# Kernel tuning notes

Measured on AMD Instinct MI355X. Metric: run time of the kernel, lower is better.

Reference implementation:

```python
import jax, jax.numpy as jnp
import numpy as np

N, E, G = 10000, 160000, 64
F, C1, C2, C3, K, NC = 128, 128, 256, 512, 5, 10


def setup_inputs() -> dict:
    key = jax.random.key(0)
    ks = jax.random.split(key, 12)
    s = 0.05
    return {
        "x": jax.random.normal(ks[0], (N, F), dtype=jnp.float32),
        "edge_index": jax.random.randint(ks[1], (2, E), 0, N, dtype=jnp.int64),
        "batch": jnp.sort(jax.random.randint(ks[2], (N,), 0, G, dtype=jnp.int64)),
        "W_cheb": jax.random.normal(ks[3], (K, F, C1), dtype=jnp.float32) * s,
        "b_cheb": jnp.zeros((C1,), jnp.float32),
        "W_g1": jax.random.normal(ks[4], (C1, C2), dtype=jnp.float32) * s,
        "b_g1": jnp.zeros((C2,), jnp.float32),
        "W_g2": jax.random.normal(ks[5], (C2, C3), dtype=jnp.float32) * s,
        "b_g2": jnp.zeros((C3,), jnp.float32),
        "w_gate": jax.random.normal(ks[6], (C3, 1), dtype=jnp.float32) * s,
        "b_gate": jnp.zeros((1,), jnp.float32),
        "W_fc": jax.random.normal(ks[7], (C3, NC), dtype=jnp.float32) * s,
        "b_fc": jnp.zeros((NC,), jnp.float32),
    }


def _deg_inv_sqrt(deg):
    return jnp.where(deg > 0, jax.lax.rsqrt(jnp.maximum(deg, 1e-12)), 0.0)


def cheb_conv(x, src, dst, W, b):
    # PyG ChebConv, sym normalization, lambda_max=2 => scaled Laplacian = -D^-1/2 A D^-1/2
    ones = jnp.ones((src.shape[0],), x.dtype)
    deg = jax.ops.segment_sum(ones, src, num_segments=N)
    dinv = _deg_inv_sqrt(deg)
    w = -(dinv[src] * dinv[dst])  # [E]

    def prop(h):
        return jax.ops.segment_sum(w[:, None] * h[src], dst, num_segments=N)

    tx0 = x
    tx1 = prop(x)
    out = tx0 @ W[0] + tx1 @ W[1]
    for k in range(2, W.shape[0]):
        tx2 = 2.0 * prop(tx1) - tx0
        out = out + tx2 @ W[k]
        tx0, tx1 = tx1, tx2
    return out + b


def gcn_conv(x, src, dst, W, b):
    # PyG GCNConv: add self-loops, sym norm D~^-1/2 (A+I) D~^-1/2, transform then aggregate
    loop = jnp.arange(N, dtype=src.dtype)
    src_a = jnp.concatenate([src, loop])
    dst_a = jnp.concatenate([dst, loop])
    ones = jnp.ones((src_a.shape[0],), x.dtype)
    deg = jax.ops.segment_sum(ones, dst_a, num_segments=N)
    dinv = _deg_inv_sqrt(deg)
    norm = dinv[src_a] * dinv[dst_a]  # [E+N]
    h = x @ W
    return jax.ops.segment_sum(norm[:, None] * h[src_a], dst_a, num_segments=N) + b


def attention_pool(x, batch, w_gate, b_gate):
    logits = (x @ w_gate + b_gate)[:, 0]  # [N]
    m = jax.ops.segment_max(logits, batch, num_segments=G)
    e = jnp.exp(logits - m[batch])
    s = jax.ops.segment_sum(e, batch, num_segments=G)
    alpha = e / s[batch]
    return jax.ops.segment_sum(alpha[:, None] * x, batch, num_segments=G)  # [G, C3]


def reference(x, edge_index, batch, W_cheb, b_cheb, W_g1, b_g1, W_g2, b_g2,
              w_gate, b_gate, W_fc, b_fc):
    src, dst = edge_index[0], edge_index[1]
    h = jax.nn.relu(cheb_conv(x, src, dst, W_cheb, b_cheb))
    h = jax.nn.relu(gcn_conv(h, src, dst, W_g1, b_g1))
    h = jax.nn.relu(gcn_conv(h, src, dst, W_g2, b_g2))
    g = attention_pool(h, batch, w_gate, b_gate)
    logits = g @ W_fc + b_fc
    return jax.nn.log_softmax(logits, axis=1)
```

## Files before the change

### kernel.cpp

```cpp
#include <hip/hip_runtime.h>
#include <hip/hip_bf16.h>
#include <math.h>

#define N_NODES 10000
#define N_EDGES 160000
#define N_GRAPHS 64
#define F_IN    128
#define C1_DIM  128
#define C2_DIM  256
#define C3_DIM  512
#define K_CHEB  5
#define NCLS    10

typedef short v8s __attribute__((ext_vector_type(8)));
typedef float v4f __attribute__((ext_vector_type(4)));

static __device__ __forceinline__ unsigned short f2bf(float f) {
    unsigned u = __float_as_uint(f);
    unsigned r = (u + 0x7FFFu + ((u >> 16) & 1u)) >> 16;
    return (unsigned short)r;
}
static __device__ __forceinline__ float bf_lo(unsigned u) { return __uint_as_float(u << 16); }
static __device__ __forceinline__ float bf_hi(unsigned u) { return __uint_as_float(u & 0xFFFF0000u); }

__global__ void count_kernel(const int* __restrict__ src, const int* __restrict__ dst,
                             int* __restrict__ cnt_s, int* __restrict__ cnt_d, int E) {
    int e = blockIdx.x * blockDim.x + threadIdx.x;
    if (e >= E) return;
    atomicAdd(&cnt_s[src[e]], 1);
    atomicAdd(&cnt_d[dst[e]], 1);
}

__global__ void dinv_kernel(const int* __restrict__ cnt_s, const int* __restrict__ cnt_d,
                            float* __restrict__ dinv_c, float* __restrict__ dinv_g, int n) {
    int i = blockIdx.x * blockDim.x + threadIdx.x;
    if (i >= n) return;
    int cs = cnt_s[i];
    dinv_c[i] = (cs > 0) ? rsqrtf((float)cs) : 0.0f;
    dinv_g[i] = rsqrtf((float)cnt_d[i] + 1.0f);
}

__global__ __launch_bounds__(256) void scan_kernel(const int* __restrict__ cnt,
                                                   int* __restrict__ rowptr, int n) {
    __shared__ int sums[256];
    int tid = threadIdx.x;
    int chunk = (n + 255) / 256;
    int s0 = tid * chunk, s1 = min(n, s0 + chunk);
    int loc = 0;
    for (int i = s0; i < s1; i++) loc += cnt[i];
    sums[tid] = loc;
    __syncthreads();
    for (int off = 1; off < 256; off <<= 1) {
        int t = (tid >= off) ? sums[tid - off] : 0;
        __syncthreads();
        sums[tid] += t;
        __syncthreads();
    }
    int pre = sums[tid] - loc;
    for (int i = s0; i < s1; i++) { rowptr[i] = pre; pre += cnt[i]; }
    if (tid == 255) rowptr[n] = pre;
}

__global__ void fill_kernel(const int* __restrict__ src, const int* __restrict__ dst,
                            const float* __restrict__ dinv_c, const float* __restrict__ dinv_g,
                            const int* __restrict__ rowptr, int* __restrict__ fillc,
                            int* __restrict__ col, float* __restrict__ wch,
                            float* __restrict__ nrm, int E) {
    int e = blockIdx.x * blockDim.x + threadIdx.x;
    if (e >= E) return;
    int s = src[e], d = dst[e];
    int pos = rowptr[d] + atomicAdd(&fillc[d], 1);
    col[pos] = s;
    wch[pos] = -(dinv_c[s] * dinv_c[d]);
    nrm[pos] = dinv_g[s] * dinv_g[d];
}

__global__ void conv_x_kernel(const float* __restrict__ x, unsigned short* __restrict__ xb,
                              unsigned short* __restrict__ tcat) {
    int id = blockIdx.x * blockDim.x + threadIdx.x;
    if (id >= N_NODES * 64) return;
    int n = id >> 6, f = (id & 63) * 2;
    float2 v = *(const float2*)(x + (size_t)n * F_IN + f);
    ushort2 o; o.x = f2bf(v.x); o.y = f2bf(v.y);
    *(ushort2*)(xb + (size_t)n * F_IN + f) = o;
    *(ushort2*)(tcat + (size_t)n * (K_CHEB * F_IN) + f) = o;
}

__global__ void wt_kernel(const float* __restrict__ Wsrc, unsigned short* __restrict__ Bt,
                          int K, int N) {
    int id = blockIdx.x * blockDim.x + threadIdx.x;
    if (id >= K * N) return;
    int n = id % N, k = id / N;
    Bt[(size_t)n * K + k] = f2bf(Wsrc[(size_t)k * N + n]);
}

__global__ __launch_bounds__(256) void gather_cheb_bf(
        const unsigned short* __restrict__ tb, const int* __restrict__ rowptr,
        const int* __restrict__ col, const float* __restrict__ ew,
        const unsigned short* __restrict__ base, float alpha, float beta,
        unsigned short* __restrict__ outc, unsigned short* __restrict__ tslice, int n) {
    int w = (blockIdx.x * blockDim.x + threadIdx.x) >> 6;
    int lane = threadIdx.x & 63;
    if (w >= n) return;
    float a0 = 0.0f, a1 = 0.0f;
    int rs = rowptr[w], re = rowptr[w + 1];
    for (int b = rs; b < re; b += 64) {
        int cl = 0; float wl = 0.0f;
        if (b + lane < re) { cl = col[b + lane]; wl = ew[b + lane]; }
        int nk4 = (min(64, re - b) + 3) & ~3;
        for (int j = 0; j < nk4; j += 4) {
            int s0 = __shfl(cl, j), s1 = __shfl(cl, j + 1);
            int s2 = __shfl(cl, j + 2), s3 = __shfl(cl, j + 3);
            float w0 = __shfl(wl, j), w1 = __shfl(wl, j + 1);
            float w2 = __shfl(wl, j + 2), w3 = __shfl(wl, j + 3);
            unsigned u0 = ((const unsigned*)(tb + (size_t)s0 * F_IN))[lane];
            unsigned u1 = ((const unsigned*)(tb + (size_t)s1 * F_IN))[lane];
            unsigned u2 = ((const unsigned*)(tb + (size_t)s2 * F_IN))[lane];
            unsigned u3 = ((const unsigned*)(tb + (size_t)s3 * F_IN))[lane];
            a0 += w0 * bf_lo(u0) + w1 * bf_lo(u1) + w2 * bf_lo(u2) + w3 * bf_lo(u3);
            a1 += w0 * bf_hi(u0) + w1 * bf_hi(u1) + w2 * bf_hi(u2) + w3 * bf_hi(u3);
        }
    }
    if (base) {
        unsigned ub = ((const unsigned*)(base + (size_t)w * F_IN))[lane];
        a0 = alpha * a0 + beta * bf_lo(ub);
        a1 = alpha * a1 + beta * bf_hi(ub);
    } else {
        a0 *= alpha; a1 *= alpha;
    }
    ushort2 o; o.x = f2bf(a0); o.y = f2bf(a1);
    *(ushort2*)(outc + (size_t)w * F_IN + lane * 2) = o;
    *(ushort2*)(tslice + (size_t)w * (K_CHEB * F_IN) + lane * 2) = o;
}

template<int FPL>
__global__ __launch_bounds__(256) void gather_gcn_pre(
        const unsigned short* __restrict__ tb, const int* __restrict__ rowptr,
        const int* __restrict__ col, const float* __restrict__ ew,
        const float* __restrict__ dinv, unsigned short* __restrict__ z, int n) {
    const int C = FPL * 64;
    int w = (blockIdx.x * blockDim.x + threadIdx.x) >> 6;
    int lane = threadIdx.x & 63;
    if (w >= n) return;
    float acc[FPL];
    #pragma unroll
    for (int q = 0; q < FPL; q++) acc[q] = 0.0f;
    int rs = rowptr[w], re = rowptr[w + 1];
    for (int b = rs; b < re; b += 64) {
        int cl = 0; float wl = 0.0f;
        if (b + lane < re) { cl = col[b + lane]; wl = ew[b + lane]; }
        int nk4 = (min(64, re - b) + 3) & ~3;
        for (int j = 0; j < nk4; j += 4) {
            int s0 = __shfl(cl, j), s1 = __shfl(cl, j + 1);
            int s2 = __shfl(cl, j + 2), s3 = __shfl(cl, j + 3);
            float w0 = __shfl(wl, j), w1 = __shfl(wl, j + 1);
            float w2 = __shfl(wl, j + 2), w3 = __shfl(wl, j + 3);
            if constexpr (FPL == 2) {
                unsigned u0 = ((const unsigned*)(tb + (size_t)s0 * C))[lane];
                unsigned u1 = ((const unsigned*)(tb + (size_t)s1 * C))[lane];
                unsigned u2 = ((const unsigned*)(tb + (size_t)s2 * C))[lane];
                unsigned u3 = ((const unsigned*)(tb + (size_t)s3 * C))[lane];
                acc[0] += w0 * bf_lo(u0) + w1 * bf_lo(u1) + w2 * bf_lo(u2) + w3 * bf_lo(u3);
                acc[1] += w0 * bf_hi(u0) + w1 * bf_hi(u1) + w2 * bf_hi(u2) + w3 * bf_hi(u3);
            } else {
                uint2 u0 = ((const uint2*)(tb + (size_t)s0 * C))[lane];
                uint2 u1 = ((const uint2*)(tb + (size_t)s1 * C))[lane];
                uint2 u2 = ((const uint2*)(tb + (size_t)s2 * C))[lane];
                uint2 u3 = ((const uint2*)(tb + (size_t)s3 * C))[lane];
                acc[0] += w0 * bf_lo(u0.x) + w1 * bf_lo(u1.x) + w2 * bf_lo(u2.x) + w3 * bf_lo(u3.x);
                acc[1] += w0 * bf_hi(u0.x) + w1 * bf_hi(u1.x) + w2 * bf_hi(u2.x) + w3 * bf_hi(u3.x);
                acc[2] += w0 * bf_lo(u0.y) + w1 * bf_lo(u1.y) + w2 * bf_lo(u2.y) + w3 * bf_lo(u3.y);
                acc[3] += w0 * bf_hi(u0.y) + w1 * bf_hi(u1.y) + w2 * bf_hi(u2.y) + w3 * bf_hi(u3.y);
            }
        }
    }
    float sn = dinv[w] * dinv[w];
    if constexpr (FPL == 2) {
        unsigned u = ((const unsigned*)(tb + (size_t)w * C))[lane];
        acc[0] += sn * bf_lo(u); acc[1] += sn * bf_hi(u);
        ushort2 o; o.x = f2bf(acc[0]); o.y = f2bf(acc[1]);
        *(ushort2*)(z + (size_t)w * C + lane * 2) = o;
    } else {
        uint2 u = ((const uint2*)(tb + (size_t)w * C))[lane];
        acc[0] += sn * bf_lo(u.x); acc[1] += sn * bf_hi(u.x);
        acc[2] += sn * bf_lo(u.y); acc[3] += sn * bf_hi(u.y);
        ushort4 o; o.x = f2bf(acc[0]); o.y = f2bf(acc[1]);
        o.z = f2bf(acc[2]); o.w = f2bf(acc[3]);
        *(ushort4*)(z + (size_t)w * C + lane * 4) = o;
    }
}

__global__ __launch_bounds__(256) void gemm_bf16(
        const unsigned short* __restrict__ A, const unsigned short* __restrict__ Bt,
        const float* __restrict__ bias, float* __restrict__ Cf,
        unsigned short* __restrict__ Cb, int M, int K, int N, int relu) {
    int m0 = blockIdx.y * 128, n0 = blockIdx.x * 128;
    int wave = threadIdx.x >> 6, lane = threadIdx.x & 63;
    int wm = (wave & 1) * 64, wn = (wave >> 1) * 64;
    int l15 = lane & 15, quad = lane >> 4;

    v4f acc[4][4];
    #pragma unroll
    for (int i = 0; i < 4; i++)
        #pragma unroll
        for (int j = 0; j < 4; j++) acc[i][j] = (v4f){0.f, 0.f, 0.f, 0.f};

    const unsigned short* Ab[4]; bool av[4];
    #pragma unroll
    for (int i = 0; i < 4; i++) {
        int row = m0 + wm + i * 16 + l15;
        av[i] = row < M;
        Ab[i] = A + (size_t)(av[i] ? row : 0) * K + quad * 8;
    }
    const unsigned short* Bb[4];
    #pragma unroll
    for (int j = 0; j < 4; j++) {
        int coln = n0 + wn + j * 16 + l15;
        Bb[j] = Bt + (size_t)coln * K + quad * 8;
    }
    const v8s zero8 = {0, 0, 0, 0, 0, 0, 0, 0};

    for (int k0 = 0; k0 < K; k0 += 32) {
        v8s a[4], b[4];
        #pragma unroll
        for (int i = 0; i < 4; i++) a[i] = av[i] ? *(const v8s*)(Ab[i] + k0) : zero8;
        #pragma unroll
        for (int j = 0; j < 4; j++) b[j] = *(const v8s*)(Bb[j] + k0);
        #pragma unroll
        for (int i = 0; i < 4; i++)
            #pragma unroll
            for (int j = 0; j < 4; j++)
                acc[i][j] = __builtin_amdgcn_mfma_f32_16x16x32_bf16(a[i], b[j], acc[i][j], 0, 0, 0);
    }

    #pragma unroll
    for (int j = 0; j < 4; j++) {
        int coln = n0 + wn + j * 16 + l15;
        float bv = bias ? bias[coln] : 0.0f;
        #pragma unroll
        for (int i = 0; i < 4; i++) {
            int rbase = m0 + wm + i * 16 + quad * 4;
            #pragma unroll
            for (int r = 0; r < 4; r++) {
                int row = rbase + r;
                if (row >= M) continue;
                float v = acc[i][j][r] + bv;
                if (relu) v = fmaxf(v, 0.0f);
                if (Cf) Cf[(size_t)row * N + coln] = v;
                else    Cb[(size_t)row * N + coln] = f2bf(v);
            }
        }
    }
}

__global__ void gate_kernel(const float* __restrict__ h3, const float* __restrict__ wg,
                            const float* __restrict__ bg, float* __restrict__ logits, int n) {
    int node = blockIdx.x * 4 + (threadIdx.x >> 6);
    int lane = threadIdx.x & 63;
    if (node >= n) return;
    float s = 0.0f;
    #pragma unroll
    for (int i = 0; i < 8; i++) {
        int c = i * 64 + lane;
        s += h3[(size_t)node * C3_DIM + c] * wg[c];
    }
    #pragma unroll
    for (int off = 32; off > 0; off >>= 1) s += __shfl_down(s, off);
    if (lane == 0) logits[node] = s + bg[0];
}

__global__ void gptr_kernel(const int* __restrict__ batch, int* __restrict__ gptr, int n) {
    int i = blockIdx.x * blockDim.x + threadIdx.x;
    if (i >= n) return;
    int b = batch[i];
    if (i == 0) { for (int g = 0; g <= b; g++) gptr[g] = 0; }
    else {
        int bp = batch[i - 1];
        for (int g = bp + 1; g <= b; g++) gptr[g] = i;
    }
    if (i == n - 1) { for (int g = b + 1; g <= N_GRAPHS; g++) gptr[g] = n; }
}

__global__ __launch_bounds__(256) void pool_stats(float* __restrict__ logits,
                                                  const int* __restrict__ gptr) {
    __shared__ float red[256];
    int g = blockIdx.x, tid = threadIdx.x;
    int gs = gptr[g], ge = gptr[g + 1];
    float m = -INFINITY;
    for (int i = gs + tid; i < ge; i += 256) m = fmaxf(m, logits[i]);
    red[tid] = m; __syncthreads();
    for (int off = 128; off > 0; off >>= 1) {
        if (tid < off) red[tid] = fmaxf(red[tid], red[tid + off]);
        __syncthreads();
    }
    m = red[0]; __syncthreads();
    float s = 0.0f;
    for (int i = gs + tid; i < ge; i += 256) s += expf(logits[i] - m);
    red[tid] = s; __syncthreads();
    for (int off = 128; off > 0; off >>= 1) {
        if (tid < off) red[tid] += red[tid + off];
        __syncthreads();
    }
    s = red[0];
    float sinv = (s > 0.0f) ? 1.0f / s : 0.0f;
    for (int i = gs + tid; i < ge; i += 256)
        logits[i] = expf(logits[i] - m) * sinv;
}

__global__ __launch_bounds__(256) void pool_partial(const float* __restrict__ h3,
        const float* __restrict__ alpha, const int* __restrict__ gptr,
        float* __restrict__ pooled) {
    int g = blockIdx.x, ch = blockIdx.y, sl = blockIdx.z;
    int gs = gptr[g], ge = gptr[g + 1];
    int cnt = ge - gs;
    int i0 = gs + (cnt * sl) / 8;
    int i1 = gs + (cnt * (sl + 1)) / 8;
    int c = ch * 256 + threadIdx.x;
    float acc = 0.0f;
    for (int i = i0; i < i1; i++)
        acc += alpha[i] * h3[(size_t)i * C3_DIM + c];
    if (i1 > i0) atomicAdd(&pooled[(size_t)g * C3_DIM + c], acc);
}

__global__ void fc_kernel(const float* __restrict__ pooled, const float* __restrict__ Wfc,
                          const float* __restrict__ bfc, float* __restrict__ out) {
    int g = blockIdx.x;
    int t = threadIdx.x;
    float acc = -INFINITY;
    if (t < NCLS) {
        acc = bfc[t];
        for (int k = 0; k < C3_DIM; k++)
            acc += pooled[(size_t)g * C3_DIM + k] * Wfc[k * NCLS + t];
    }
    float m = acc;
    #pragma unroll
    for (int off = 8; off > 0; off >>= 1) m = fmaxf(m, __shfl_xor(m, off, 16));
    float e = (t < NCLS) ? expf(acc - m) : 0.0f;
    float s = e;
    #pragma unroll
    for (int off = 8; off > 0; off >>= 1) s += __shfl_xor(s, off, 16);
    if (t < NCLS) out[g * NCLS + t] = acc - m - logf(s);
}

extern "C" void kernel_launch(void* const* d_in, const int* in_sizes, int n_in,
                              void* d_out, int out_size, void* d_ws, size_t ws_size,
                              hipStream_t stream) {
    const float* x      = (const float*)d_in[0];
    const int*   ei     = (const int*)d_in[1];
    const int*   batch  = (const int*)d_in[2];
    const float* W_cheb = (const float*)d_in[3];
    const float* b_cheb = (const float*)d_in[4];
    const float* W_g1   = (const float*)d_in[5];
    const float* b_g1   = (const float*)d_in[6];
    const float* W_g2   = (const float*)d_in[7];
    const float* b_g2   = (const float*)d_in[8];
    const float* w_gate = (const float*)d_in[9];
    const float* b_gate = (const float*)d_in[10];
    const float* W_fc   = (const float*)d_in[11];
    const float* b_fc   = (const float*)d_in[12];
    const int* src = ei;
    const int* dst = ei + N_EDGES;
    float* out = (float*)d_out;

    const int N = N_NODES, E = N_EDGES, G = N_GRAPHS;

    char* Wp = (char*)d_ws;
    auto alloc = [&](size_t bytes) {
        void* p = Wp;
        Wp += (bytes + 255) & ~(size_t)255;
        return p;
    };
    int*   cnt_s   = (int*)alloc(N * 4);
    int*   cnt_d   = (int*)alloc(N * 4);
    int*   fillc   = (int*)alloc(N * 4);
    int*   rowptr  = (int*)alloc((N + 1) * 4);
    int*   col     = (int*)alloc(E * 4);
    float* wch     = (float*)alloc(E * 4);
    float* nrm     = (float*)alloc(E * 4);
    float* dinv_c  = (float*)alloc(N * 4);
    float* dinv_g  = (float*)alloc(N * 4);
    unsigned short* xb    = (unsigned short*)alloc((size_t)N * F_IN * 2);
    unsigned short* t1b   = (unsigned short*)alloc((size_t)N * F_IN * 2);
    unsigned short* t2b   = (unsigned short*)alloc((size_t)N * F_IN * 2);
    unsigned short* t3b   = (unsigned short*)alloc((size_t)N * F_IN * 2);
    unsigned short* t4b   = (unsigned short*)alloc((size_t)N * F_IN * 2);
    unsigned short* tcat  = (unsigned short*)alloc((size_t)N * K_CHEB * F_IN * 2);
    unsigned short* h1b   = (unsigned short*)alloc((size_t)N * C1_DIM * 2);
    unsigned short* z1b   = (unsigned short*)alloc((size_t)N * C1_DIM * 2);
    unsigned short* h2b   = (unsigned short*)alloc((size_t)N * C2_DIM * 2);
    unsigned short* z2b   = (unsigned short*)alloc((size_t)N * C2_DIM * 2);
    float* h3      = (float*)alloc((size_t)N * C3_DIM * 4);
    unsigned short* Wcb_t = (unsigned short*)alloc((size_t)K_CHEB * F_IN * C1_DIM * 2);
    unsigned short* Wg1_t = (unsigned short*)alloc((size_t)C1_DIM * C2_DIM * 2);
    unsigned short* Wg2_t = (unsigned short*)alloc((size_t)C2_DIM * C3_DIM * 2);
    float* logits  = (float*)alloc(N * 4);
    int*   gptr    = (int*)alloc((G + 1) * 4);
    float* pooled  = (float*)alloc((size_t)G * C3_DIM * 4);

    dim3 blk(256);
    auto cdiv = [](int a, int b) { return (a + b - 1) / b; };

    hipMemsetAsync(cnt_s, 0, N * sizeof(int), stream);
    hipMemsetAsync(cnt_d, 0, N * sizeof(int), stream);
    hipMemsetAsync(fillc, 0, N * sizeof(int), stream);
    hipLaunchKernelGGL(count_kernel, dim3(cdiv(E, 256)), blk, 0, stream, src, dst, cnt_s, cnt_d, E);
    hipLaunchKernelGGL(dinv_kernel, dim3(cdiv(N, 256)), blk, 0, stream, cnt_s, cnt_d, dinv_c, dinv_g, N);
    hipLaunchKernelGGL(scan_kernel, dim3(1), blk, 0, stream, cnt_d, rowptr, N);
    hipLaunchKernelGGL(fill_kernel, dim3(cdiv(E, 256)), blk, 0, stream,
                       src, dst, dinv_c, dinv_g, rowptr, fillc, col, wch, nrm, E);

    hipLaunchKernelGGL(conv_x_kernel, dim3(cdiv(N * 64, 256)), blk, 0, stream, x, xb, tcat);
    hipLaunchKernelGGL(wt_kernel, dim3(cdiv(K_CHEB * F_IN * C1_DIM, 256)), blk, 0, stream,
                       W_cheb, Wcb_t, K_CHEB * F_IN, C1_DIM);
    hipLaunchKernelGGL(wt_kernel, dim3(cdiv(C1_DIM * C2_DIM, 256)), blk, 0, stream,
                       W_g1, Wg1_t, C1_DIM, C2_DIM);
    hipLaunchKernelGGL(wt_kernel, dim3(cdiv(C2_DIM * C3_DIM, 256)), blk, 0, stream,
                       W_g2, Wg2_t, C2_DIM, C3_DIM);

    const int NWB = cdiv(N, 4);
    const int TC = K_CHEB * F_IN;

    hipLaunchKernelGGL(gather_cheb_bf, dim3(NWB), blk, 0, stream,
                       xb, rowptr, col, wch, (const unsigned short*)nullptr, 1.0f, 0.0f,
                       t1b, tcat + 1 * F_IN, N);
    hipLaunchKernelGGL(gather_cheb_bf, dim3(NWB), blk, 0, stream,
                       t1b, rowptr, col, wch, xb, 2.0f, -1.0f, t2b, tcat + 2 * F_IN, N);
    hipLaunchKernelGGL(gather_cheb_bf, dim3(NWB), blk, 0, stream,
                       t2b, rowptr, col, wch, t1b, 2.0f, -1.0f, t3b, tcat + 3 * F_IN, N);
    hipLaunchKernelGGL(gather_cheb_bf, dim3(NWB), blk, 0, stream,
                       t3b, rowptr, col, wch, t2b, 2.0f, -1.0f, t4b, tcat + 4 * F_IN, N);

    hipLaunchKernelGGL(gemm_bf16, dim3(C1_DIM / 128, cdiv(N, 128)), blk, 0, stream,
                       tcat, Wcb_t, b_cheb, (float*)nullptr, h1b, N, TC, C1_DIM, 1);

    hipLaunchKernelGGL(gather_gcn_pre<2>, dim3(NWB), blk, 0, stream,
                       h1b, rowptr, col, nrm, dinv_g, z1b, N);
    hipLaunchKernelGGL(gemm_bf16, dim3(C2_DIM / 128, cdiv(N, 128)), blk, 0, stream,
                       z1b, Wg1_t, b_g1, (float*)nullptr, h2b, N, C1_DIM, C2_DIM, 1);

    hipLaunchKernelGGL(gather_gcn_pre<4>, dim3(NWB), blk, 0, stream,
                       h2b, rowptr, col, nrm, dinv_g, z2b, N);
    hipLaunchKernelGGL(gemm_bf16, dim3(C3_DIM / 128, cdiv(N, 128)), blk, 0, stream,
                       z2b, Wg2_t, b_g2, h3, (unsigned short*)nullptr, N, C2_DIM, C3_DIM, 1);

    hipLaunchKernelGGL(gate_kernel, dim3(cdiv(N, 4)), blk, 0, stream, h3, w_gate, b_gate, logits, N);
    hipLaunchKernelGGL(gptr_kernel, dim3(cdiv(N, 256)), blk, 0, stream, batch, gptr, N);
    hipLaunchKernelGGL(pool_stats, dim3(G), blk, 0, stream, logits, gptr);
    hipMemsetAsync(pooled, 0, (size_t)G * C3_DIM * sizeof(float), stream);
    hipLaunchKernelGGL(pool_partial, dim3(G, C3_DIM / 256, 8), blk, 0, stream,
                       h3, logits, gptr, pooled);

    hipLaunchKernelGGL(fc_kernel, dim3(G), dim3(64), 0, stream, pooled, W_fc, b_fc, out);
}
```

Measured before the change: 320.1 us.

## Merge prep kernels, gather Chebyshev terms in place, shrink GEMM M-tile

Folds the x conversion, the three weight transposes and the graph-pointer build into one prep kernel, and merges the dinv computation into the scan kernel. The memsets are consolidated, and the pooled buffer is now zeroed inside pool_stats. The Chebyshev gathers read and write directly in the concatenated tcat buffer at stride TC, which drops the separate t1..t4 buffers and the duplicate store. The GEMM tile height goes from 128 to 64 rows, giving twice as many blocks for better occupancy on a 10000-row problem, at the cost of less B reuse per block. Reading from the strided tcat buffer may reduce cache locality in the gathers.

```diff
diff --git a/kernel.cpp b/kernel.cpp
--- a/kernel.cpp
+++ b/kernel.cpp
@@ -11,6 +11,7 @@
 #define C3_DIM  512
 #define K_CHEB  5
 #define NCLS    10
+#define TC      (K_CHEB * F_IN)
 
 typedef short v8s __attribute__((ext_vector_type(8)));
 typedef float v4f __attribute__((ext_vector_type(4)));
@@ -31,23 +32,21 @@
     atomicAdd(&cnt_d[dst[e]], 1);
 }
 
-__global__ void dinv_kernel(const int* __restrict__ cnt_s, const int* __restrict__ cnt_d,
-                            float* __restrict__ dinv_c, float* __restrict__ dinv_g, int n) {
-    int i = blockIdx.x * blockDim.x + threadIdx.x;
-    if (i >= n) return;
-    int cs = cnt_s[i];
-    dinv_c[i] = (cs > 0) ? rsqrtf((float)cs) : 0.0f;
-    dinv_g[i] = rsqrtf((float)cnt_d[i] + 1.0f);
-}
-
-__global__ __launch_bounds__(256) void scan_kernel(const int* __restrict__ cnt,
-                                                   int* __restrict__ rowptr, int n) {
+__global__ __launch_bounds__(256) void scan_dinv_kernel(
+        const int* __restrict__ cnt_s, const int* __restrict__ cnt_d,
+        int* __restrict__ rowptr, float* __restrict__ dinv_c, float* __restrict__ dinv_g, int n) {
     __shared__ int sums[256];
     int tid = threadIdx.x;
     int chunk = (n + 255) / 256;
     int s0 = tid * chunk, s1 = min(n, s0 + chunk);
     int loc = 0;
-    for (int i = s0; i < s1; i++) loc += cnt[i];
+    for (int i = s0; i < s1; i++) {
+        int cd = cnt_d[i];
+        loc += cd;
+        int cs = cnt_s[i];
+        dinv_c[i] = (cs > 0) ? rsqrtf((float)cs) : 0.0f;
+        dinv_g[i] = rsqrtf((float)cd + 1.0f);
+    }
     sums[tid] = loc;
     __syncthreads();
     for (int off = 1; off < 256; off <<= 1) {
@@ -57,7 +56,7 @@
         __syncthreads();
     }
     int pre = sums[tid] - loc;
-    for (int i = s0; i < s1; i++) { rowptr[i] = pre; pre += cnt[i]; }
+    for (int i = s0; i < s1; i++) { rowptr[i] = pre; pre += cnt_d[i]; }
     if (tid == 255) rowptr[n] = pre;
 }
 
@@ -75,30 +74,61 @@
     nrm[pos] = dinv_g[s] * dinv_g[d];
 }
 
-__global__ void conv_x_kernel(const float* __restrict__ x, unsigned short* __restrict__ xb,
-                              unsigned short* __restrict__ tcat) {
+#define PREP_A (N_NODES * 64)
+#define PREP_B (TC * C1_DIM)
+#define PREP_C (C1_DIM * C2_DIM)
+#define PREP_D (C2_DIM * C3_DIM)
+#define PREP_TOTAL (PREP_A + PREP_B + PREP_C + PREP_D + N_NODES)
+__global__ void prep_kernel(const float* __restrict__ x, unsigned short* __restrict__ tcat,
+                            const float* __restrict__ Wcheb, unsigned short* __restrict__ Wcb_t,
+                            const float* __restrict__ Wg1, unsigned short* __restrict__ Wg1_t,
+                            const float* __restrict__ Wg2, unsigned short* __restrict__ Wg2_t,
+                            const int* __restrict__ batch, int* __restrict__ gptr) {
     int id = blockIdx.x * blockDim.x + threadIdx.x;
-    if (id >= N_NODES * 64) return;
-    int n = id >> 6, f = (id & 63) * 2;
-    float2 v = *(const float2*)(x + (size_t)n * F_IN + f);
-    ushort2 o; o.x = f2bf(v.x); o.y = f2bf(v.y);
-    *(ushort2*)(xb + (size_t)n * F_IN + f) = o;
-    *(ushort2*)(tcat + (size_t)n * (K_CHEB * F_IN) + f) = o;
-}
-
-__global__ void wt_kernel(const float* __restrict__ Wsrc, unsigned short* __restrict__ Bt,
-                          int K, int N) {
-    int id = blockIdx.x * blockDim.x + threadIdx.x;
-    if (id >= K * N) return;
-    int n = id % N, k = id / N;
-    Bt[(size_t)n * K + k] = f2bf(Wsrc[(size_t)k * N + n]);
+    if (id < PREP_A) {
+        int n = id >> 6, f = (id & 63) * 2;
+        float2 v = *(const float2*)(x + (size_t)n * F_IN + f);
+        ushort2 o; o.x = f2bf(v.x); o.y = f2bf(v.y);
+        *(ushort2*)(tcat + (size_t)n * TC + f) = o;
+        return;
+    }
+    id -= PREP_A;
+    if (id < PREP_B) {
+        int n = id % C1_DIM, k = id / C1_DIM;
+        Wcb_t[(size_t)n * TC + k] = f2bf(Wcheb[(size_t)k * C1_DIM + n]);
+        return;
+    }
+    id -= PREP_B;
+    if (id < PREP_C) {
+        int n = id % C2_DIM, k = id / C2_DIM;
+        Wg1_t[(size_t)n * C1_DIM + k] = f2bf(Wg1[(size_t)k * C2_DIM + n]);
+        return;
+    }
+    id -= PREP_C;
+    if (id < PREP_D) {
+        int n = id % C3_DIM, k = id / C3_DIM;
+        Wg2_t[(size_t)n * C2_DIM + k] = f2bf(Wg2[(size_t)k * C3_DIM + n]);
+        return;
+    }
+    id -= PREP_D;
+    int i = id;
+    int b = batch[i];
+    if (i == 0) { for (int g = 0; g <= b; g++) gptr[g] = 0; }
+    else {
+        int bp = batch[i - 1];
+        for (int g = bp + 1; g <= b; g++) gptr[g] = i;
+    }
+    if (i == N_NODES - 1) { for (int g = b + 1; g <= N_GRAPHS; g++) gptr[g] = N_NODES; }
 }
 
 __global__ __launch_bounds__(256) void gather_cheb_bf(
-        const unsigned short* __restrict__ tb, const int* __restrict__ rowptr,
-        const int* __restrict__ col, const float* __restrict__ ew,
-        const unsigned short* __restrict__ base, float alpha, float beta,
-        unsigned short* __restrict__ outc, unsigned short* __restrict__ tslice, int n) {
+        const unsigned short* __restrict__ tb,
+        const int* __restrict__ rowptr, const int* __restrict__ col,
+        const float* __restrict__ ew,
+        const unsigned short* __restrict__ base,
+        float alpha, float beta,
+        unsigned short* __restrict__ outc,
+        int n) {
     int w = (blockIdx.x * blockDim.x + threadIdx.x) >> 6;
     int lane = threadIdx.x & 63;
     if (w >= n) return;
@@ -113,24 +143,23 @@
             int s2 = __shfl(cl, j + 2), s3 = __shfl(cl, j + 3);
             float w0 = __shfl(wl, j), w1 = __shfl(wl, j + 1);
             float w2 = __shfl(wl, j + 2), w3 = __shfl(wl, j + 3);
-            unsigned u0 = ((const unsigned*)(tb + (size_t)s0 * F_IN))[lane];
-            unsigned u1 = ((const unsigned*)(tb + (size_t)s1 * F_IN))[lane];
-            unsigned u2 = ((const unsigned*)(tb + (size_t)s2 * F_IN))[lane];
-            unsigned u3 = ((const unsigned*)(tb + (size_t)s3 * F_IN))[lane];
+            unsigned u0 = ((const unsigned*)(tb + (size_t)s0 * TC))[lane];
+            unsigned u1 = ((const unsigned*)(tb + (size_t)s1 * TC))[lane];
+            unsigned u2 = ((const unsigned*)(tb + (size_t)s2 * TC))[lane];
+            unsigned u3 = ((const unsigned*)(tb + (size_t)s3 * TC))[lane];
             a0 += w0 * bf_lo(u0) + w1 * bf_lo(u1) + w2 * bf_lo(u2) + w3 * bf_lo(u3);
             a1 += w0 * bf_hi(u0) + w1 * bf_hi(u1) + w2 * bf_hi(u2) + w3 * bf_hi(u3);
         }
     }
     if (base) {
-        unsigned ub = ((const unsigned*)(base + (size_t)w * F_IN))[lane];
+        unsigned ub = ((const unsigned*)(base + (size_t)w * TC))[lane];
         a0 = alpha * a0 + beta * bf_lo(ub);
         a1 = alpha * a1 + beta * bf_hi(ub);
     } else {
         a0 *= alpha; a1 *= alpha;
     }
     ushort2 o; o.x = f2bf(a0); o.y = f2bf(a1);
-    *(ushort2*)(outc + (size_t)w * F_IN + lane * 2) = o;
-    *(ushort2*)(tslice + (size_t)w * (K_CHEB * F_IN) + lane * 2) = o;
+    *(ushort2*)(outc + (size_t)w * TC + lane * 2) = o;
 }
 
 template<int FPL>
@@ -194,20 +223,20 @@
         const unsigned short* __restrict__ A, const unsigned short* __restrict__ Bt,
         const float* __restrict__ bias, float* __restrict__ Cf,
         unsigned short* __restrict__ Cb, int M, int K, int N, int relu) {
-    int m0 = blockIdx.y * 128, n0 = blockIdx.x * 128;
+    int m0 = blockIdx.y * 64, n0 = blockIdx.x * 128;
     int wave = threadIdx.x >> 6, lane = threadIdx.x & 63;
-    int wm = (wave & 1) * 64, wn = (wave >> 1) * 64;
+    int wm = (wave & 1) * 32, wn = (wave >> 1) * 64;
     int l15 = lane & 15, quad = lane >> 4;
 
-    v4f acc[4][4];
-    #pragma unroll
-    for (int i = 0; i < 4; i++)
+    v4f acc[2][4];
+    #pragma unroll
+    for (int i = 0; i < 2; i++)
         #pragma unroll
         for (int j = 0; j < 4; j++) acc[i][j] = (v4f){0.f, 0.f, 0.f, 0.f};
 
-    const unsigned short* Ab[4]; bool av[4];
-    #pragma unroll
-    for (int i = 0; i < 4; i++) {
+    const unsigned short* Ab[2]; bool av[2];
+    #pragma unroll
+    for (int i = 0; i < 2; i++) {
         int row = m0 + wm + i * 16 + l15;
         av[i] = row < M;
         Ab[i] = A + (size_t)(av[i] ? row : 0) * K + quad * 8;
@@ -221,13 +250,13 @@
     const v8s zero8 = {0, 0, 0, 0, 0, 0, 0, 0};
 
     for (int k0 = 0; k0 < K; k0 += 32) {
-        v8s a[4], b[4];
+        v8s a[2], b[4];
         #pragma unroll
-        for (int i = 0; i < 4; i++) a[i] = av[i] ? *(const v8s*)(Ab[i] + k0) : zero8;
+        for (int i = 0; i < 2; i++) a[i] = av[i] ? *(const v8s*)(Ab[i] + k0) : zero8;
         #pragma unroll
         for (int j = 0; j < 4; j++) b[j] = *(const v8s*)(Bb[j] + k0);
         #pragma unroll
-        for (int i = 0; i < 4; i++)
+        for (int i = 0; i < 2; i++)
             #pragma unroll
             for (int j = 0; j < 4; j++)
                 acc[i][j] = __builtin_amdgcn_mfma_f32_16x16x32_bf16(a[i], b[j], acc[i][j], 0, 0, 0);
@@ -238,7 +267,7 @@
         int coln = n0 + wn + j * 16 + l15;
         float bv = bias ? bias[coln] : 0.0f;
         #pragma unroll
-        for (int i = 0; i < 4; i++) {
+        for (int i = 0; i < 2; i++) {
             int rbase = m0 + wm + i * 16 + quad * 4;
             #pragma unroll
             for (int r = 0; r < 4; r++) {
@@ -269,23 +298,14 @@
     if (lane == 0) logits[node] = s + bg[0];
 }
 
-__global__ void gptr_kernel(const int* __restrict__ batch, int* __restrict__ gptr, int n) {
-    int i = blockIdx.x * blockDim.x + threadIdx.x;
-    if (i >= n) return;
-    int b = batch[i];
-    if (i == 0) { for (int g = 0; g <= b; g++) gptr[g] = 0; }
-    else {
-        int bp = batch[i - 1];
-        for (int g = bp + 1; g <= b; g++) gptr[g] = i;
-    }
-    if (i == n - 1) { for (int g = b + 1; g <= N_GRAPHS; g++) gptr[g] = n; }
-}
-
 __global__ __launch_bounds__(256) void pool_stats(float* __restrict__ logits,
-                                                  const int* __restrict__ gptr) {
+                                                  const int* __restrict__ gptr,
+                                                  float* __restrict__ pooled) {
     __shared__ float red[256];
     int g = blockIdx.x, tid = threadIdx.x;
     int gs = gptr[g], ge = gptr[g + 1];
+    pooled[(size_t)g * C3_DIM + tid] = 0.0f;
+    pooled[(size_t)g * C3_DIM + 256 + tid] = 0.0f;
     float m = -INFINITY;
     for (int i = gs + tid; i < ge; i += 256) m = fmaxf(m, logits[i]);
     red[tid] = m; __syncthreads();
@@ -370,27 +390,23 @@
         Wp += (bytes + 255) & ~(size_t)255;
         return p;
     };
-    int*   cnt_s   = (int*)alloc(N * 4);
-    int*   cnt_d   = (int*)alloc(N * 4);
-    int*   fillc   = (int*)alloc(N * 4);
+    int*   cnt3    = (int*)alloc((size_t)3 * N * 4);
+    int*   cnt_s   = cnt3;
+    int*   cnt_d   = cnt3 + N;
+    int*   fillc   = cnt3 + 2 * N;
     int*   rowptr  = (int*)alloc((N + 1) * 4);
     int*   col     = (int*)alloc(E * 4);
     float* wch     = (float*)alloc(E * 4);
     float* nrm     = (float*)alloc(E * 4);
     float* dinv_c  = (float*)alloc(N * 4);
     float* dinv_g  = (float*)alloc(N * 4);
-    unsigned short* xb    = (unsigned short*)alloc((size_t)N * F_IN * 2);
-    unsigned short* t1b   = (unsigned short*)alloc((size_t)N * F_IN * 2);
-    unsigned short* t2b   = (unsigned short*)alloc((size_t)N * F_IN * 2);
-    unsigned short* t3b   = (unsigned short*)alloc((size_t)N * F_IN * 2);
-    unsigned short* t4b   = (unsigned short*)alloc((size_t)N * F_IN * 2);
-    unsigned short* tcat  = (unsigned short*)alloc((size_t)N * K_CHEB * F_IN * 2);
+    unsigned short* tcat  = (unsigned short*)alloc((size_t)N * TC * 2);
     unsigned short* h1b   = (unsigned short*)alloc((size_t)N * C1_DIM * 2);
     unsigned short* z1b   = (unsigned short*)alloc((size_t)N * C1_DIM * 2);
     unsigned short* h2b   = (unsigned short*)alloc((size_t)N * C2_DIM * 2);
     unsigned short* z2b   = (unsigned short*)alloc((size_t)N * C2_DIM * 2);
     float* h3      = (float*)alloc((size_t)N * C3_DIM * 4);
-    unsigned short* Wcb_t = (unsigned short*)alloc((size_t)K_CHEB * F_IN * C1_DIM * 2);
+    unsigned short* Wcb_t = (unsigned short*)alloc((size_t)TC * C1_DIM * 2);
     unsigned short* Wg1_t = (unsigned short*)alloc((size_t)C1_DIM * C2_DIM * 2);
     unsigned short* Wg2_t = (unsigned short*)alloc((size_t)C2_DIM * C3_DIM * 2);
     float* logits  = (float*)alloc(N * 4);
@@ -400,53 +416,45 @@
     dim3 blk(256);
     auto cdiv = [](int a, int b) { return (a + b - 1) / b; };
 
-    hipMemsetAsync(cnt_s, 0, N * sizeof(int), stream);
-    hipMemsetAsync(cnt_d, 0, N * sizeof(int), stream);
-    hipMemsetAsync(fillc, 0, N * sizeof(int), stream);
+    hipLaunchKernelGGL(prep_kernel, dim3(cdiv(PREP_TOTAL, 256)), blk, 0, stream,
+                       x, tcat, W_cheb, Wcb_t, W_g1, Wg1_t, W_g2, Wg2_t, batch, gptr);
+
+    hipMemsetAsync(cnt3, 0, (size_t)3 * N * sizeof(int), stream);
     hipLaunchKernelGGL(count_kernel, dim3(cdiv(E, 256)), blk, 0, stream, src, dst, cnt_s, cnt_d, E);
-    hipLaunchKernelGGL(dinv_kernel, dim3(cdiv(N, 256)), blk, 0, stream, cnt_s, cnt_d, dinv_c, dinv_g, N);
-    hipLaunchKernelGGL(scan_kernel, dim3(1), blk, 0, stream, cnt_d, rowptr, N);
+    hipLaunchKernelGGL(scan_dinv_kernel, dim3(1), blk, 0, stream, cnt_s, cnt_d, rowptr, dinv_c, dinv_g, N);
     hipLaunchKernelGGL(fill_kernel, dim3(cdiv(E, 256)), blk, 0, stream,
                        src, dst, dinv_c, dinv_g, rowptr, fillc, col, wch, nrm, E);
 
-    hipLaunchKernelGGL(conv_x_kernel, dim3(cdiv(N * 64, 256)), blk, 0, stream, x, xb, tcat);
-    hipLaunchKernelGGL(wt_kernel, dim3(cdiv(K_CHEB * F_IN * C1_DIM, 256)), blk, 0, stream,
-                       W_cheb, Wcb_t, K_CHEB * F_IN, C1_DIM);
-    hipLaunchKernelGGL(wt_kernel, dim3(cdiv(C1_DIM * C2_DIM, 256)), blk, 0, stream,
-                       W_g1, Wg1_t, C1_DIM, C2_DIM);
-    hipLaunchKernelGGL(wt_kernel, dim3(cdiv(C2_DIM * C3_DIM, 256)), blk, 0, stream,
-                       W_g2, Wg2_t, C2_DIM, C3_DIM);
-
     const int NWB = cdiv(N, 4);
-    const int TC = K_CHEB * F_IN;
 
     hipLaunchKernelGGL(gather_cheb_bf, dim3(NWB), blk, 0, stream,
-                       xb, rowptr, col, wch, (const unsigned short*)nullptr, 1.0f, 0.0f,
-                       t1b, tcat + 1 * F_IN, N);
+                       tcat + 0 * F_IN, rowptr, col, wch,
+                       (const unsigned short*)nullptr, 1.0f, 0.0f, tcat + 1 * F_IN, N);
     hipLaunchKernelGGL(gather_cheb_bf, dim3(NWB), blk, 0, stream,
-                       t1b, rowptr, col, wch, xb, 2.0f, -1.0f, t2b, tcat + 2 * F_IN, N);
+                       tcat + 1 * F_IN, rowptr, col, wch,
+                       tcat + 0 * F_IN, 2.0f, -1.0f, tcat + 2 * F_IN, N);
     hipLaunchKernelGGL(gather_cheb_bf, dim3(NWB), blk, 0, stream,
-                       t2b, rowptr, col, wch, t1b, 2.0f, -1.0f, t3b, tcat + 3 * F_IN, N);
+                       tcat + 2 * F_IN, rowptr, col, wch,
+                       tcat + 1 * F_IN, 2.0f, -1.0f, tcat + 3 * F_IN, N);
     hipLaunchKernelGGL(gather_cheb_bf, dim3(NWB), blk, 0, stream,
-                       t3b, rowptr, col, wch, t2b, 2.0f, -1.0f, t4b, tcat + 4 * F_IN, N);
-
-    hipLaunchKernelGGL(gemm_bf16, dim3(C1_DIM / 128, cdiv(N, 128)), blk, 0, stream,
+                       tcat + 3 * F_IN, rowptr, col, wch,
+                       tcat + 2 * F_IN, 2.0f, -1.0f, tcat + 4 * F_IN, N);
+
+    hipLaunchKernelGGL(gemm_bf16, dim3(C1_DIM / 128, cdiv(N, 64)), blk, 0, stream,
                        tcat, Wcb_t, b_cheb, (float*)nullptr, h1b, N, TC, C1_DIM, 1);
 
     hipLaunchKernelGGL(gather_gcn_pre<2>, dim3(NWB), blk, 0, stream,
                        h1b, rowptr, col, nrm, dinv_g, z1b, N);
-    hipLaunchKernelGGL(gemm_bf16, dim3(C2_DIM / 128, cdiv(N, 128)), blk, 0, stream,
+    hipLaunchKernelGGL(gemm_bf16, dim3(C2_DIM / 128, cdiv(N, 64)), blk, 0, stream,
                        z1b, Wg1_t, b_g1, (float*)nullptr, h2b, N, C1_DIM, C2_DIM, 1);
 
     hipLaunchKernelGGL(gather_gcn_pre<4>, dim3(NWB), blk, 0, stream,
                        h2b, rowptr, col, nrm, dinv_g, z2b, N);
-    hipLaunchKernelGGL(gemm_bf16, dim3(C3_DIM / 128, cdiv(N, 128)), blk, 0, stream,
+    hipLaunchKernelGGL(gemm_bf16, dim3(C3_DIM / 128, cdiv(N, 64)), blk, 0, stream,
                        z2b, Wg2_t, b_g2, h3, (unsigned short*)nullptr, N, C2_DIM, C3_DIM, 1);
 
     hipLaunchKernelGGL(gate_kernel, dim3(cdiv(N, 4)), blk, 0, stream, h3, w_gate, b_gate, logits, N);
-    hipLaunchKernelGGL(gptr_kernel, dim3(cdiv(N, 256)), blk, 0, stream, batch, gptr, N);
-    hipLaunchKernelGGL(pool_stats, dim3(G), blk, 0, stream, logits, gptr);
-    hipMemsetAsync(pooled, 0, (size_t)G * C3_DIM * sizeof(float), stream);
+    hipLaunchKernelGGL(pool_stats, dim3(G), blk, 0, stream, logits, gptr, pooled);
     hipLaunchKernelGGL(pool_partial, dim3(G, C3_DIM / 256, 8), blk, 0, stream,
                        h3, logits, gptr, pooled);
 
```

Result: faster. 312.6 us (-2.3%).
